# Kernel optimization log

Hardware: AMD Instinct MI355X
Metric: run time of the kernel (lower is better)

## Reference

```python
import jax, jax.numpy as jnp
import numpy as np

FRACTION_BITS = 16
INTEGER_BITS = 16
DELTA = 2.0 ** (-(FRACTION_BITS / 2))  # 2^-8
BOUND = 2.0 ** (INTEGER_BITS - 1)      # 2^15


def round_to_fixed(x):
    # floor(x/delta + 0.5), clipped to [-2^15, 2^15-1], rescaled
    rounded = jnp.floor(x / DELTA + 0.5)
    return jnp.clip(rounded, -BOUND, BOUND - 1) * DELTA


def setup_inputs() -> dict:
    key = jax.random.key(0)
    k_x, k_sh, k_sg, k_b = jax.random.split(key, 4)
    N, IN, OUT = 8192, 4096, 4096
    x = jax.random.normal(k_x, (N, IN), dtype=jnp.float32)
    shift = jax.random.uniform(k_sh, (OUT, IN), minval=-10.0, maxval=-1.0, dtype=jnp.float32)
    sign = jax.random.uniform(k_sg, (OUT, IN), minval=-1.0, maxval=0.0, dtype=jnp.float32)
    bound = 1.0 / np.sqrt(IN)
    bias = jax.random.uniform(k_b, (OUT,), minval=-bound, maxval=bound, dtype=jnp.float32)
    return {"x": x, "shift": shift, "sign": sign, "bias": bias}


def reference(x, shift, sign, bias):
    # fixed-point quantization of activations and bias (fallback float path)
    x_q = round_to_fixed(x)
    b_q = round_to_fixed(bias)
    # power-of-two weight: v = 2^round(shift) * (-1)^round(sign)
    v = jnp.exp2(jnp.round(shift)) * jnp.where(jnp.round(sign) % 2 == 0, 1.0, -1.0)
    out = x_q @ v.T + b_q[None, :]
    return out
```

## Files before the change

### kernel.cpp

```cpp
#include <hip/hip_runtime.h>


typedef _Float16 half8 __attribute__((ext_vector_type(8)));
typedef _Float16 half4v __attribute__((ext_vector_type(4)));
typedef float floatx4 __attribute__((ext_vector_type(4)));

__device__ __forceinline__ float qfix(float x) {
    float r = floorf(x * 256.0f + 0.5f);
    r = fminf(fmaxf(r, -32768.0f), 32767.0f);
    return r * 0.00390625f;
}

__global__ __launch_bounds__(256) void quantize_x_kernel(
        const float* __restrict__ x, _Float16* __restrict__ xq, int n4) {
    int i = blockIdx.x * 256 + threadIdx.x;
    const int stride = gridDim.x * 256;
    for (; i < n4; i += stride) {
        float4 v = reinterpret_cast<const float4*>(x)[i];
        half4v o;
        o[0] = (_Float16)qfix(v.x);
        o[1] = (_Float16)qfix(v.y);
        o[2] = (_Float16)qfix(v.z);
        o[3] = (_Float16)qfix(v.w);
        reinterpret_cast<half4v*>(xq)[i] = o;
    }
}

__global__ __launch_bounds__(256) void make_v_kernel(
        const float* __restrict__ shift, const float* __restrict__ sign,
        _Float16* __restrict__ v, int n4) {
    int i = blockIdx.x * 256 + threadIdx.x;
    const int stride = gridDim.x * 256;
    for (; i < n4; i += stride) {
        float4 sh = reinterpret_cast<const float4*>(shift)[i];
        float4 sg = reinterpret_cast<const float4*>(sign)[i];
        half4v o;
        o[0] = (_Float16)ldexpf((rintf(sg.x) == 0.0f) ? 1.0f : -1.0f, (int)rintf(sh.x));
        o[1] = (_Float16)ldexpf((rintf(sg.y) == 0.0f) ? 1.0f : -1.0f, (int)rintf(sh.y));
        o[2] = (_Float16)ldexpf((rintf(sg.z) == 0.0f) ? 1.0f : -1.0f, (int)rintf(sh.z));
        o[3] = (_Float16)ldexpf((rintf(sg.w) == 0.0f) ? 1.0f : -1.0f, (int)rintf(sh.w));
        reinterpret_cast<half4v*>(v)[i] = o;
    }
}

__device__ __forceinline__ void async_load16(const void* g, void* l) {
    __builtin_amdgcn_global_lo\
ad_lds(
        (const __attribute__((address_space(1))) unsigned int*)g,
        (__attribute__((address_space(3))) unsigned int*)l,
        16, 0, 0);
}

#define STAGE(P, DST) async_load16((P), (DST) + t * 8)

#define STAGE_TILE(NS)  do {                                              \
    STAGE(pA0, (NS));            STAGE(pB0, (NS) + 8192);                 \
    STAGE(pB1, (NS) + 12288);    STAGE(pA1, (NS) + 4096);                 \
    pA0 += 32; pA1 += 32; pB0 += 32; pB1 += 32; } while (0)

#define VM8()  asm volatile("s_waitcnt vmcnt(8)" ::: "memory")
#define VM4()  asm volatile("s_waitcnt vmcnt(4)" ::: "memory")
#define VM0()  asm volatile("s_waitcnt vmcnt(0)" ::: "memory")
#define BAR()  do { asm volatile("" ::: "memory");                        \
                    __builtin_amdgcn_s_barrier();                         \
                    asm volatile("" ::: "memory"); } while (0)

__global__ __launch_bounds__(512, 2) void gemm8_kernel(
        const _Float16* __restrict__ A,
        const _Float16* __restrict__ B,
        const float* __restrict__ bias,
        float* __restrict__ C,
        int M, int N, int K) {
    extern __shared__ _Float16 smem[];
    const int t = threadIdx.x;
    const int lane = t & 63;
    const int w = t >> 6;
    const int wrow = w >> 2;
    const int wcol = w & 3;
    const int fr  = lane & 15;
    const int kb  = lane >> 4;

    const int nwg = gridDim.x;
    const int bid = blockIdx.x;
    const int cpx = nwg >> 3;
    const int swz = (bid & 7) * cpx + (bid >> 3);
    const int ntN = N >> 8;
    const int bm = (swz / ntN) << 8;
    const int bn = (swz % ntN) << 8;

    const int r0  = t >> 2;
    const int cbo = ((t & 3) ^ ((t >> 3) & 3)) * 8;
    const _Float16* pA0 = A + (size_t)(bm +       r0) * K + cbo;
    const _Float16* pA1 = A + (size_t)(bm + 128 + r0) * K + cbo;
    const _Float16* pB0 = B + (size_t)(bn +       r0) * K + cbo;
    const _Float16* pB1 = B + (size_t)(bn + 128 + r0) * K + cbo;

    const int xk = ((kb ^ ((fr >> 1) & 3)) << 4);
    const char* sbase = (const char*)smem;
    const char* aRow = sbase + (wrow * 64 + fr) * 64 + xk;
    const char* bR0  = sbase + 16384 + (wcol * 32 +      fr) * 64 + xk;
    const char* bR1  = sbase + 16384 + (wcol * 32 + 16 + fr) * 64 + xk;

    STAGE_TILE(smem);
    STAGE_TILE(smem + 16384);
    STAGE_TILE(smem + 32768);
    VM8();

    floatx4 acc[2][2][4][2] = {};
    const int NT = K >> 5;

    for (int T = 0; T < NT; ++T) {
        BAR();
        const int sb = (T & 3) << 15;

        half8 af0[4], af1[4], bf0[2], bf1[2];
        #pragma unroll
        for (int mf = 0; mf < 4; ++mf) {
            af0[mf] = *reinterpret_cast<const half8*>(aRow + sb +        mf * 1024);
            af1[mf] = *reinterpret_cast<const half8*>(aRow + sb + 8192 + mf * 1024);
        }
        bf0[0] = *reinterpret_cast<const half8*>(bR0 + sb);
        bf0[1] = *reinterpret_cast<const half8*>(bR1 + sb);
        bf1[0] = *reinterpret_cast<const half8*>(bR0 + sb + 8192);
        bf1[1] = *reinterpret_cast<const half8*>(bR1 + sb + 8192);

        if (T < NT - 3)
            STAGE_TILE(smem + (((T + 3) & 3) << 14));

        #pragma unroll
        for (int mf = 0; mf < 4; ++mf)
          #pragma unroll
          for (int nf = 0; nf < 2; ++nf) {
            acc[0][0][mf][nf] = __builtin_amdgcn_mfma_f32_16x16x32_f16(
                af0[mf], bf0[nf], acc[0][0][mf][nf], 0, 0, 0);
            acc[0][1][mf][nf] = __builtin_amdgcn_mfma_f32_16x16x32_f16(
                af0[mf], bf1[nf], acc[0][1][mf][nf], 0, 0, 0);
            acc[1][1][mf][nf] = __builtin_amdgcn_mfma_f32_16x16x32_f16(
                af1[mf], bf1[nf], acc[1][1][mf][nf], 0, 0, 0);
            acc[1][0][mf][nf] = __builtin_amdgcn_mfma_f32_16x16x32_f16(
                af1[mf], bf0[nf], acc[1][0][mf][nf], 0, 0, 0);
          }

        if (T < NT - 3)      { VM8(); }
        else if (T == NT - 3){ VM4(); }
        else if (T == NT - 2){ VM0(); }
    }

    #pragma unroll
    for (int qm = 0; qm < 2; ++qm)
      #pragma unroll
      for (int qn = 0; qn < 2; ++qn)
        #pragma unroll
        for (int nf = 0; nf < 2; ++nf) {
            const int gcol = bn + qn * 128 + wcol * 32 + nf * 16 + (lane & 15);
            const float bq = qfix(bias[gcol]);
            #pragma unroll
            for (int mf = 0; mf < 4; ++mf) {
                const int grow = bm + qm * 128 + wrow * 64 + mf * 16 + ((lane >> 4) << 2);
                float* p = C + (size_t)grow * N + gcol;
                #pragma unroll
                for (int r = 0; r < 4; ++r)
                    p[(size_t)r * N] = acc[qm][qn][mf][nf][r] + bq;
            }
        }
}

extern "C" void kernel_launch(void* const* d_in, const int* in_sizes, int n_in,
                              void* d_out, int out_size, void* d_ws, size_t ws_size,
                              hipStream_t stream) {
    const float* x     = (const float*)d_in[0];
    const float* shift = (const float*)d_in[1];
    const float* sign  = (const float*)d_in[2];
    const float* bias  = (const float*)d_in[3];
    float* out = (float*)d_out;

    const int N = in_sizes[3];
    const int K = in_sizes[1] / N;
    const int M = in_sizes[0] / K;

    _Float16* xq = (_Float16*)d_ws;
    _Float16* v  = (_Float16*)((char*)d_ws + (size_t)M * K * sizeof(_Float16));

    quantize_x_kernel<<<2048, 256, 0, stream>>>(x, xq, M * K / 4);
    make_v_kernel<<<2048, 256, 0, stream>>>(shift, sign, v, N * K / 4);

    (void)hipFuncSetAttribute(reinterpret_cast<const void*>(gemm8_kernel),
                              hipFuncAttributeMaxDynamicSharedMemorySize, 131072);
    const int nblk = (M / 256) * (N / 256);
    gemm8_kernel<<<nblk, 512, 131072, stream>>>(xq, v, bias, out, M, N, K);
}
```

Before: 306.3 us.

## Software-pipeline LDS fragment reads across K-tiles with double-buffered registers

Unrolls the GEMM K-loop by two and double-buffers the A and B fragment registers. The fragments for the next K-tile are read from shared memory while the MFMAs for the current tile run, and the wait count is relaxed to vmcnt(4). The goal is to hide LDS read latency behind matrix instructions and cut stalls between barriers. In exchange it holds more live fragment registers alongside the large accumulator set, which risks spilling or lower occupancy.

```diff
diff --git a/kernel.cpp b/kernel.cpp
--- a/kernel.cpp
+++ b/kernel.cpp
@@ -44,26 +44,48 @@
 }
 
 __device__ __forceinline__ void async_load16(const void* g, void* l) {
-    __builtin_amdgcn_global_lo\
-ad_lds(
+    __builtin_amdgcn_global_load_lds(
         (const __attribute__((address_space(1))) unsigned int*)g,
         (__attribute__((address_space(3))) unsigned int*)l,
         16, 0, 0);
 }
 
 #define STAGE(P, DST) async_load16((P), (DST) + t * 8)
-
 #define STAGE_TILE(NS)  do {                                              \
     STAGE(pA0, (NS));            STAGE(pB0, (NS) + 8192);                 \
     STAGE(pB1, (NS) + 12288);    STAGE(pA1, (NS) + 4096);                 \
     pA0 += 32; pA1 += 32; pB0 += 32; pB1 += 32; } while (0)
 
-#define VM8()  asm volatile("s_waitcnt vmcnt(8)" ::: "memory")
 #define VM4()  asm volatile("s_waitcnt vmcnt(4)" ::: "memory")
 #define VM0()  asm volatile("s_waitcnt vmcnt(0)" ::: "memory")
+#define VM8()  asm volatile("s_waitcnt vmcnt(8)" ::: "memory")
 #define BAR()  do { asm volatile("" ::: "memory");                        \
                     __builtin_amdgcn_s_barrier();                         \
                     asm volatile("" ::: "memory"); } while (0)
+
+#define READ_AFQ(DST, SB, Q)                                              \
+    _Pragma("unroll")                                                     \
+    for (int mf = 0; mf < 4; ++mf)                                        \
+      DST[mf] = *reinterpret_cast<const half8*>(                          \
+          aRow + (SB) + (Q) * 8192 + mf * 1024);
+
+#define READ_BF4(DST, SB)                                                 \
+    do {                                                                  \
+      DST[0] = *reinterpret_cast<const half8*>(bR0 + (SB));               \
+      DST[1] = *reinterpret_cast<const half8*>(bR1 + (SB));               \
+      DST[2] = *reinterpret_cast<const half8*>(bR0 + (SB) + 8192);        \
+      DST[3] = *reinterpret_cast<const half8*>(bR1 + (SB) + 8192);        \
+    } while (0)
+
+#define MFMA16(QM, AF, BF)                                                \
+    _Pragma("unroll")                                                     \
+    for (int qn = 0; qn < 2; ++qn)                                        \
+      _Pragma("unroll")                                                   \
+      for (int mf = 0; mf < 4; ++mf)                                      \
+        _Pragma("unroll")                                                 \
+        for (int nf = 0; nf < 2; ++nf)                                    \
+          acc[QM][qn][mf][nf] = __builtin_amdgcn_mfma_f32_16x16x32_f16(   \
+              AF[mf], BF[qn * 2 + nf], acc[QM][qn][mf][nf], 0, 0, 0);
 
 __global__ __launch_bounds__(512, 2) void gemm8_kernel(
         const _Float16* __restrict__ A,
@@ -105,45 +127,41 @@
     STAGE_TILE(smem + 16384);
     STAGE_TILE(smem + 32768);
     VM8();
+    BAR();
+
+    half8 afA[4], afB[4], bfC[4], bfN[4];
+    READ_AFQ(afA, 0, 0);
+    READ_BF4(bfC, 0);
 
     floatx4 acc[2][2][4][2] = {};
     const int NT = K >> 5;
 
-    for (int T = 0; T < NT; ++T) {
-        BAR();
-        const int sb = (T & 3) << 15;
-
-        half8 af0[4], af1[4], bf0[2], bf1[2];
-        #pragma unroll
-        for (int mf = 0; mf < 4; ++mf) {
-            af0[mf] = *reinterpret_cast<const half8*>(aRow + sb +        mf * 1024);
-            af1[mf] = *reinterpret_cast<const half8*>(aRow + sb + 8192 + mf * 1024);
+    for (int T = 0; T < NT; T += 2) {
+        {
+            if (T < NT - 2) { VM4(); } else { VM0(); }
+            BAR();
+            const int sb0 = (T & 3) << 15;
+            const int sb1 = ((T + 1) & 3) << 15;
+            READ_AFQ(afB, sb0, 1);
+            READ_BF4(bfN, sb1);
+            MFMA16(0, afA, bfC);
+            READ_AFQ(afA, sb1, 0);
+            if (T + 3 < NT) STAGE_TILE(smem + (((T + 3) & 3) << 14));
+            MFMA16(1, afB, bfC);
         }
-        bf0[0] = *reinterpret_cast<const half8*>(bR0 + sb);
-        bf0[1] = *reinterpret_cast<const half8*>(bR1 + sb);
-        bf1[0] = *reinterpret_cast<const half8*>(bR0 + sb + 8192);
-        bf1[1] = *reinterpret_cast<const half8*>(bR1 + sb + 8192);
-
-        if (T < NT - 3)
-            STAGE_TILE(smem + (((T + 3) & 3) << 14));
-
-        #pragma unroll
-        for (int mf = 0; mf < 4; ++mf)
-          #pragma unroll
-          for (int nf = 0; nf < 2; ++nf) {
-            acc[0][0][mf][nf] = __builtin_amdgcn_mfma_f32_16x16x32_f16(
-                af0[mf], bf0[nf], acc[0][0][mf][nf], 0, 0, 0);
-            acc[0][1][mf][nf] = __builtin_amdgcn_mfma_f32_16x16x32_f16(
-                af0[mf], bf1[nf], acc[0][1][mf][nf], 0, 0, 0);
-            acc[1][1][mf][nf] = __builtin_amdgcn_mfma_f32_16x16x32_f16(
-                af1[mf], bf1[nf], acc[1][1][mf][nf], 0, 0, 0);
-            acc[1][0][mf][nf] = __builtin_amdgcn_mfma_f32_16x16x32_f16(
-                af1[mf], bf0[nf], acc[1][0][mf][nf], 0, 0, 0);
-          }
-
-        if (T < NT - 3)      { VM8(); }
-        else if (T == NT - 3){ VM4(); }
-        else if (T == NT - 2){ VM0(); }
+        {
+            const int T1 = T + 1;
+            if (T1 < NT - 2) { VM4(); } else if (T1 == NT - 2) { VM0(); }
+            BAR();
+            const int sb1 = (T1 & 3) << 15;
+            const int sb2 = ((T1 + 1) & 3) << 15;
+            READ_AFQ(afB, sb1, 1);
+            if (T1 + 1 < NT) READ_BF4(bfC, sb2);
+            MFMA16(0, afA, bfN);
+            if (T1 + 1 < NT) READ_AFQ(afA, sb2, 0);
+            if (T1 + 3 < NT) STAGE_TILE(smem + (((T1 + 3) & 3) << 14));
+            MFMA16(1, afB, bfN);
+        }
     }
 
     #pragma unroll
```

After: 319.7 us. 1.04x slower.

## Switch GEMM inner loop to 32x32x16 MFMA with remapped warp tiles

Applied to the files above, without the earlier changes.

Replaces the 16x16x32 MFMA tiling (split quadrants per wave) with 32x32x16 MFMA instructions, so each wave owns a contiguous 128x64 output block built from 4x2 tiles of 32x32. LDS fragment addressing and the epilogue store mapping are rebuilt for the 32x32 accumulator layout. The waitcnt inline asm is swapped for builtins. The aim is fewer MFMA issues and fewer LDS fragment reads per FLOP. In exchange, each wave holds larger accumulators and the LDS access pattern changes, which could add bank conflicts.

```diff
diff --git a/kernel.cpp b/kernel.cpp
--- a/kernel.cpp
+++ b/kernel.cpp
@@ -3,7 +3,7 @@
 
 typedef _Float16 half8 __attribute__((ext_vector_type(8)));
 typedef _Float16 half4v __attribute__((ext_vector_type(4)));
-typedef float floatx4 __attribute__((ext_vector_type(4)));
+typedef float floatx16 __attribute__((ext_vector_type(16)));
 
 __device__ __forceinline__ float qfix(float x) {
     float r = floorf(x * 256.0f + 0.5f);
@@ -44,26 +44,23 @@
 }
 
 __device__ __forceinline__ void async_load16(const void* g, void* l) {
-    __builtin_amdgcn_global_lo\
-ad_lds(
+    __builtin_amdgcn_global_load_lds(
         (const __attribute__((address_space(1))) unsigned int*)g,
         (__attribute__((address_space(3))) unsigned int*)l,
         16, 0, 0);
 }
 
 #define STAGE(P, DST) async_load16((P), (DST) + t * 8)
-
 #define STAGE_TILE(NS)  do {                                              \
     STAGE(pA0, (NS));            STAGE(pB0, (NS) + 8192);                 \
     STAGE(pB1, (NS) + 12288);    STAGE(pA1, (NS) + 4096);                 \
     pA0 += 32; pA1 += 32; pB0 += 32; pB1 += 32; } while (0)
 
-#define VM8()  asm volatile("s_waitcnt vmcnt(8)" ::: "memory")
-#define VM4()  asm volatile("s_waitcnt vmcnt(4)" ::: "memory")
-#define VM0()  asm volatile("s_waitcnt vmcnt(0)" ::: "memory")
-#define BAR()  do { asm volatile("" ::: "memory");                        \
-                    __builtin_amdgcn_s_barrier();                         \
-                    asm volatile("" ::: "memory"); } while (0)
+#define FENCE() asm volatile("" ::: "memory")
+#define VM8()  do { FENCE(); __builtin_amdgcn_s_waitcnt(0x0F78); FENCE(); } while (0)
+#define VM4()  do { FENCE(); __builtin_amdgcn_s_waitcnt(0x0F74); FENCE(); } while (0)
+#define VM0()  do { FENCE(); __builtin_amdgcn_s_waitcnt(0x0F70); FENCE(); } while (0)
+#define BAR()  do { FENCE(); __builtin_amdgcn_s_barrier(); FENCE(); } while (0)
 
 __global__ __launch_bounds__(512, 2) void gemm8_kernel(
         const _Float16* __restrict__ A,
@@ -77,8 +74,8 @@
     const int w = t >> 6;
     const int wrow = w >> 2;
     const int wcol = w & 3;
-    const int fr  = lane & 15;
-    const int kb  = lane >> 4;
+    const int fr32 = lane & 31;
+    const int hi   = lane >> 5;
 
     const int nwg = gridDim.x;
     const int bid = blockIdx.x;
@@ -95,51 +92,49 @@
     const _Float16* pB0 = B + (size_t)(bn +       r0) * K + cbo;
     const _Float16* pB1 = B + (size_t)(bn + 128 + r0) * K + cbo;
 
-    const int xk = ((kb ^ ((fr >> 1) & 3)) << 4);
+    const int key = (fr32 >> 1) & 3;
+    const int xk0 = (((0 << 1) + hi) ^ key) << 4;
+    const int xk1 = (((1 << 1) + hi) ^ key) << 4;
     const char* sbase = (const char*)smem;
-    const char* aRow = sbase + (wrow * 64 + fr) * 64 + xk;
-    const char* bR0  = sbase + 16384 + (wcol * 32 +      fr) * 64 + xk;
-    const char* bR1  = sbase + 16384 + (wcol * 32 + 16 + fr) * 64 + xk;
+    const char* aRow = sbase + wrow * 8192 + fr32 * 64;
+    const char* bRow = sbase + 16384 + (wcol >> 1) * 8192
+                             + ((wcol & 1) * 64 + fr32) * 64;
 
     STAGE_TILE(smem);
     STAGE_TILE(smem + 16384);
     STAGE_TILE(smem + 32768);
     VM8();
 
-    floatx4 acc[2][2][4][2] = {};
+    floatx16 acc[4][2] = {};
     const int NT = K >> 5;
 
     for (int T = 0; T < NT; ++T) {
         BAR();
         const int sb = (T & 3) << 15;
 
-        half8 af0[4], af1[4], bf0[2], bf1[2];
+        half8 af[4][2], bf[2][2];
         #pragma unroll
-        for (int mf = 0; mf < 4; ++mf) {
-            af0[mf] = *reinterpret_cast<const half8*>(aRow + sb +        mf * 1024);
-            af1[mf] = *reinterpret_cast<const half8*>(aRow + sb + 8192 + mf * 1024);
+        for (int rt = 0; rt < 4; ++rt) {
+            af[rt][0] = *reinterpret_cast<const half8*>(aRow + sb + rt * 2048 + xk0);
+            af[rt][1] = *reinterpret_cast<const half8*>(aRow + sb + rt * 2048 + xk1);
         }
-        bf0[0] = *reinterpret_cast<const half8*>(bR0 + sb);
-        bf0[1] = *reinterpret_cast<const half8*>(bR1 + sb);
-        bf1[0] = *reinterpret_cast<const half8*>(bR0 + sb + 8192);
-        bf1[1] = *reinterpret_cast<const half8*>(bR1 + sb + 8192);
+        #pragma unroll
+        for (int ct = 0; ct < 2; ++ct) {
+            bf[ct][0] = *reinterpret_cast<const half8*>(bRow + sb + ct * 2048 + xk0);
+            bf[ct][1] = *reinterpret_cast<const half8*>(bRow + sb + ct * 2048 + xk1);
+        }
 
         if (T < NT - 3)
             STAGE_TILE(smem + (((T + 3) & 3) << 14));
 
         #pragma unroll
-        for (int mf = 0; mf < 4; ++mf)
+        for (int rt = 0; rt < 4; ++rt)
           #pragma unroll
-          for (int nf = 0; nf < 2; ++nf) {
-            acc[0][0][mf][nf] = __builtin_amdgcn_mfma_f32_16x16x32_f16(
-                af0[mf], bf0[nf], acc[0][0][mf][nf], 0, 0, 0);
-            acc[0][1][mf][nf] = __builtin_amdgcn_mfma_f32_16x16x32_f16(
-                af0[mf], bf1[nf], acc[0][1][mf][nf], 0, 0, 0);
-            acc[1][1][mf][nf] = __builtin_amdgcn_mfma_f32_16x16x32_f16(
-                af1[mf], bf1[nf], acc[1][1][mf][nf], 0, 0, 0);
-            acc[1][0][mf][nf] = __builtin_amdgcn_mfma_f32_16x16x32_f16(
-                af1[mf], bf0[nf], acc[1][0][mf][nf], 0, 0, 0);
-          }
+          for (int ct = 0; ct < 2; ++ct)
+            #pragma unroll
+            for (int ks = 0; ks < 2; ++ks)
+              acc[rt][ct] = __builtin_amdgcn_mfma_f32_32x32x16_f16(
+                  af[rt][ks], bf[ct][ks], acc[rt][ct], 0, 0, 0);
 
         if (T < NT - 3)      { VM8(); }
         else if (T == NT - 3){ VM4(); }
@@ -147,22 +142,18 @@
     }
 
     #pragma unroll
-    for (int qm = 0; qm < 2; ++qm)
+    for (int rt = 0; rt < 4; ++rt)
       #pragma unroll
-      for (int qn = 0; qn < 2; ++qn)
-        #pragma unroll
-        for (int nf = 0; nf < 2; ++nf) {
-            const int gcol = bn + qn * 128 + wcol * 32 + nf * 16 + (lane & 15);
-            const float bq = qfix(bias[gcol]);
-            #pragma unroll
-            for (int mf = 0; mf < 4; ++mf) {
-                const int grow = bm + qm * 128 + wrow * 64 + mf * 16 + ((lane >> 4) << 2);
-                float* p = C + (size_t)grow * N + gcol;
-                #pragma unroll
-                for (int r = 0; r < 4; ++r)
-                    p[(size_t)r * N] = acc[qm][qn][mf][nf][r] + bq;
-            }
-        }
+      for (int ct = 0; ct < 2; ++ct) {
+          const int gcol = bn + wcol * 64 + ct * 32 + fr32;
+          const float bq = qfix(bias[gcol]);
+          const int grow0 = bm + wrow * 128 + rt * 32 + (hi << 2);
+          #pragma unroll
+          for (int r = 0; r < 16; ++r) {
+              const int grow = grow0 + (r & 3) + ((r >> 2) << 3);
+              C[(size_t)grow * N + gcol] = acc[rt][ct][r] + bq;
+          }
+      }
 }
 
 extern "C" void kernel_launch(void* const* d_in, const int* in_sizes, int n_in,
```

Result: slower. 323.6 us (+5.6%).
